# Kernel optimization log

Hardware: AMD Instinct MI355X
Metric: run time of the kernel (lower is better)

Reference implementation:

```python
import jax, jax.numpy as jnp
import numpy as np

ALPHA = 0.2          # LeakyReLU negative slope (Alpha)
NEG_INF = -9e15      # mask value used by pygat-style GAT


def _masked_attention(Wh, a_src, a_dst, mask):
    """Wh: [H,N,d], a_src/a_dst: [H,d], mask: [N,N] (nonzero = edge).
    Returns attention-aggregated features [H,N,d]."""
    f_src = jnp.einsum('hnd,hd->hn', Wh, a_src)   # [H,N]
    f_dst = jnp.einsum('hnd,hd->hn', Wh, a_dst)   # [H,N]
    e = jax.nn.leaky_relu(f_src[:, :, None] + f_dst[:, None, :], ALPHA)  # [H,N,N]
    e = jnp.where(mask[None, :, :] > 0, e, NEG_INF)
    att = jax.nn.softmax(e, axis=-1)              # masked softmax over neighbors
    return jnp.einsum('hnm,hmd->hnd', att, Wh)    # [H,N,d]


def setup_inputs() -> dict:
    key = jax.random.key(0)
    ks = jax.random.split(key, 8)
    N, F_in, D, H = 4096, 512, 64, 8
    x = jax.random.normal(ks[0], (N, F_in), dtype=jnp.float32)
    adj = jax.random.randint(ks[1], (N, N), 0, 2, dtype=jnp.int32)
    s = 0.1
    W = jax.random.normal(ks[2], (H, F_in, D), dtype=jnp.float32) * s
    a_src = jax.random.normal(ks[3], (H, D), dtype=jnp.float32) * s
    a_dst = jax.random.normal(ks[4], (H, D), dtype=jnp.float32) * s
    W_o = jax.random.normal(ks[5], (H * D, D), dtype=jnp.float32) * s
    ao_src = jax.random.normal(ks[6], (D,), dtype=jnp.float32) * s
    ao_dst = jax.random.normal(ks[7], (D,), dtype=jnp.float32) * s
    return {"x": x, "adj": adj, "W": W, "a_src": a_src, "a_dst": a_dst,
            "W_o": W_o, "ao_src": ao_src, "ao_dst": ao_dst}


def reference(x, adj, W, a_src, a_dst, W_o, ao_src, ao_dst):
    N = x.shape[0]
    # --- multi-head layer (concat=True: ELU per head, concat on feature dim) ---
    Wh = jnp.einsum('nf,hfd->hnd', x, W)                     # [H,N,d]
    h1 = jax.nn.elu(_masked_attention(Wh, a_src, a_dst, adj))  # [H,N,d]
    h_cat = jnp.transpose(h1, (1, 0, 2)).reshape(N, -1)      # [N, H*d]
    # --- output head (concat=False: no ELU inside layer) ---
    Who = (h_cat @ W_o)[None]                                # [1,N,d]
    h2 = _masked_attention(Who, ao_src[None], ao_dst[None], adj)[0]  # [N,d]
    # GAT.forward: activation (ELU) then log_softmax over dim=1
    return jax.nn.log_softmax(jax.nn.elu(h2), axis=1)
```

## Files before the change

### kernel.cpp

```cpp
#include <hip/hip_runtime.h>
#include <hip/hip_bf16.h>
#include <math.h>

#define N_NODES 4096
#define FDIM 512
#define D 64
#define H 8
#define NWORDS (N_NODES / 64)

typedef __attribute__((ext_vector_type(8))) short bf16x8;
typedef __attribute__((ext_vector_type(4))) float f32x4;

__device__ inline short f2bf(float x) {
    return (short)((__builtin_bit_cast(unsigned int, x) + 0x8000u) >> 16);
}

__device__ inline int sext_bit(unsigned int v, int j) {
#if defined(__has_builtin) && __has_builtin(__builtin_amdgcn_sbfe)
    return __builtin_amdgcn_sbfe((int)v, j, 1);
#else
    return ((int)(v << (31 - j))) >> 31;
#endif
}

__device__ inline unsigned fenc(float f) {
    unsigned u = __builtin_bit_cast(unsigned, f);
    return (u & 0x80000000u) ? ~u : (u | 0x80000000u);
}
__device__ inline float fdec(unsigned e) {
    unsigned u = (e & 0x80000000u) ? (e & 0x7FFFFFFFu) : ~e;
    return __builtin_bit_cast(float, u);
}

__device__ inline void gl2lds16(const void* g, void* l) {
#if defined(__has_builtin) && __has_builtin(__builtin_amdgcn_global_load_lds)
    __builtin_amdgcn_global_load_lds(
        (const __attribute__((address_space(1))) unsigned int*)g,
        (__attribute__((address_space(3))) unsigned int*)l, 16, 0, 0);
#else
    *(uint4*)l = *(const uint4*)g;
#endif
}

#define NB_BITS (N_NODES * N_NODES / 256)
#define NB_X    (N_NODES * FDIM / 256)
#define NB_W    (H * FDIM * D / 256)
#define NB_WO   (FDIM * D / 256)
__global__ void k_pre(const int* __restrict__ adj, const float* __restrict__ x,
                      const float* __restrict__ W, const float* __restrict__ Wo,
                      unsigned long long* __restrict__ bits, short* __restrict__ Xbf,
                      short* __restrict__ WF, short* __restrict__ WoF,
                      float* __restrict__ cm1, float* __restrict__ cm2,
                      unsigned* __restrict__ gmaxe1, unsigned* __restrict__ gmaxe2) {
    const int b = blockIdx.x, t = threadIdx.x;
    if (b == 0) {
        for (int i = t; i < H * D; i += 256) cm1[i] = 0.f;
        if (t < D) cm2[t] = 0.f;
        if (t < H) gmaxe1[t] = 0u;
        if (t == 0) gmaxe2[0] = 0u;
        return;
    }
    if (b < 1 + NB_BITS) {
        const int idx = (b - 1) * 256 + t;
        unsigned long long m = __ballot(adj[idx] != 0);
        if ((t & 63) == 0) bits[idx >> 6] = m;
        return;
    }
    if (b < 1 + NB_BITS + NB_X) {
        const size_t idx = (size_t)(b - 1 - NB_BITS) * 256 + t;
        Xbf[idx] = f2bf(x[idx]);
        return;
    }
    if (b < 1 + NB_BITS + NB_X + NB_W) {
        const size_t idx = (size_t)(b - 1 - NB_BITS - NB_X) * 256 + t;
        const int d = idx & 63;
        const int k = (int)(idx >> 6) & 511;
        const int h = (int)(idx >> 15);
        WF[(((size_t)h * 64 + (k >> 3)) * 64 + d) * 8 + (k & 7)] = f2bf(W[idx]);
        return;
    }
    {
        const size_t idx = (size_t)(b - 1 - NB_BITS - NB_X - NB_W) * 256 + t;
        const int d = idx & 63;
        const int k = (int)(idx >> 6);
        WoF[(((size_t)(k >> 3)) * 64 + d) * 8 + (k & 7)] = f2bf(Wo[idx]);
    }
}

__global__ void __launch_bounds__(256) k_gemm(
    const short* __restrict__ Xbf, const short* __restrict__ WF,
    const float* __restrict__ av, const float* __restrict__ bv,
    short* __restrict__ WBout, float* __restrict__ fs, float* __restrict__ fd,
    unsigned* __restrict__ gmaxe, float* __restrict__ cm) {
    const int h  = blockIdx.y;
    const int i0 = blockIdx.x * 64;
    const int t = threadIdx.x, w = t >> 6, lane = t & 63;
    const int li = lane & 15, quad = lane >> 4, k0 = quad * 8;
    const int row_a = i0 + w * 16 + li;
    const short* __restrict__ Xr  = Xbf + (size_t)row_a * FDIM;
    const short* __restrict__ WFh = WF + (size_t)h * 64 * D * 8;

    f32x4 c0 = {0.f, 0.f, 0.f, 0.f}, c1 = c0, c2 = c0, c3 = c0;
    #pragma unroll 4
    for (int kt = 0; kt < FDIM; kt += 32) {
        bf16x8 a = *(const bf16x8*)&Xr[kt + k0];
        const short* bb = WFh + (size_t)((kt >> 3) + quad) * (D * 8) + li * 8;
        bf16x8 b0 = *(const bf16x8*)(bb);
        bf16x8 b1 = *(const bf16x8*)(bb + 128);
        bf16x8 b2 = *(const bf16x8*)(bb + 256);
        bf16x8 b3 = *(const bf16x8*)(bb + 384);
        c0 = __builtin_amdgcn_mfma_f32_16x16x32_bf16(a, b0, c0, 0, 0, 0);
        c1 = __builtin_amdgcn_mfma_f32_16x16x32_bf16(a, b1, c1, 0, 0, 0);
        c2 = __builtin_amdgcn_mfma_f32_16x16x32_bf16(a, b2, c2, 0, 0, 0);
        c3 = __builtin_amdgcn_mfma_f32_16x16x32_bf16(a, b3, c3, 0, 0, 0);
    }
    float av4[4], bv4[4];
    #pragma unroll
    for (int t4 = 0; t4 < 4; ++t4) {
        av4[t4] = av[h * D + t4 * 16 + li];
        bv4[t4] = bv[h * D + t4 * 16 + li];
    }
    float tiles[4][4];
    #pragma unroll
    for (int r = 0; r < 4; ++r) { tiles[0][r] = c0[r]; tiles[1][r] = c1[r]; tiles[2][r] = c2[r]; tiles[3][r] = c3[r]; }

    __shared__ float csum[4][64];
    __shared__ float red[4];
    float fdmax = -INFINITY;
    float s4[4] = {0.f, 0.f, 0.f, 0.f};

    #pragma unroll
    for (int r = 0; r < 4; ++r) {
        const int row = i0 + w * 16 + quad * 4 + r;
        float pa = 0.f, pb = 0.f;
        #pragma unroll
        for (int t4 = 0; t4 < 4; ++t4) {
            const float v = tiles[t4][r];
            const int d = t4 * 16 + li;
            WBout[((size_t)h * (N_NODES / 8) + (row >> 3)) * (D * 8) + d * 8 + (row & 7)] = f2bf(v);
            pa += v * av4[t4];
            pb += v * bv4[t4];
            s4[t4] += v;
        }
        #pragma unroll
        for (int off = 1; off < 16; off <<= 1) {
            pa += __shfl_xor(pa, off);
            pb += __shfl_xor(pb, off);
        }
        if (li == 0) {
            fs[(size_t)h * N_NODES + row] = pa;
            fd[(size_t)h * N_NODES + row] = pb;
        }
        fdmax = fmaxf(fdmax, pb);
    }
    fdmax = fmaxf(fdmax, __shfl_xor(fdmax, 16));
    fdmax = fmaxf(fdmax, __shfl_xor(fdmax, 32));
    if (lane == 0) red[w] = fdmax;
    #pragma unroll
    for (int t4 = 0; t4 < 4; ++t4) {
        s4[t4] += __shfl_xor(s4[t4], 16);
        s4[t4] += __shfl_xor(s4[t4], 32);
    }
    if (quad == 0)
        #pragma unroll
        for (int t4 = 0; t4 < 4; ++t4) csum[w][t4 * 16 + li] = s4[t4];
    __syncthreads();
    if (t == 0)
        atomicMax(gmaxe + h, fenc(fmaxf(fmaxf(red[0], red[1]), fmaxf(red[2], red[3]))));
    if (t < 64)
        atomicAdd(&cm[h * D + t],
                  (csum[0][t] + csum[1][t] + csum[2][t] + csum[3][t]) * (1.f / (float)N_NODES));
}

__global__ void __launch_bounds__(256) k_accum(
    const unsigned int* __restrict__ bits32,
    const short* __restrict__ WB,
    const float* __restrict__ fsb, const float* __restrict__ fdb,
    const unsigned* __restrict__ gmaxe,
    float* __restrict__ num, float* __restrict__ den, int kslab) {

    __shared__ __align__(16) short Bt[2][16 * 64 * 8];
    __shared__ __align__(16) float EG[2][256];

    const int h = blockIdx.y, i0 = blockIdx.x * 128, slab = blockIdx.z;
    const int t = threadIdx.x, w = t >> 6, lane = t & 63;
    const int li = lane & 15, quad = lane >> 4, k0 = quad * 8;
    const int    r0 = i0 + w * 32 + li;
    const int    r1 = r0 + 16;
    const size_t ho = (size_t)h * N_NODES;
    const float  gm = fdec(gmaxe[h]);
    const float  Rv0 = __expf(-0.8f * (fsb[ho + r0] + gm));
    const float  Rv1 = __expf(-0.8f * (fsb[ho + r1] + gm));
    const float* __restrict__ fd = fdb + ho;
    const short* __restrict__ Bh = WB + (size_t)h * (N_NODES / 8) * D * 8;
    const unsigned int* __restrict__ brow0 = bits32 + (size_t)r0 * (NWORDS * 2);
    const unsigned int* __restrict__ brow1 = bits32 + (size_t)r1 * (NWORDS * 2);

    f32x4 acc[2][4], c5[2];
    #pragma unroll
    for (int f = 0; f < 2; ++f) {
        #pragma unroll
        for (int q = 0; q < 4; ++q) acc[f][q] = (f32x4){0.f, 0.f, 0.f, 0.f};
        c5[f] = (f32x4){0.f, 0.f, 0.f, 0.f};
    }
    bf16x8 ones;
    #pragma unroll
    for (int j = 0; j < 8; ++j) ones[j] = (short)0x3F80;

    const int k_beg = slab * kslab;
    const int ntile = kslab / 128;

    auto stage = [&](int buf, int jt) {
        const short* src = Bh + (size_t)(jt >> 3) * (D * 8);
        #pragma unroll
        for (int p = 0; p < 4; ++p)
            gl2lds16(src + (size_t)(p * 256 + t) * 8, &Bt[buf][(p * 256 + t) * 8]);
        if (w == 0) {
            float2 f2 = *(const float2*)&fd[jt + lane * 2];
            float2 ev, gv;
            ev.x = __expf(f2.x - gm);          ev.y = __expf(f2.y - gm);
            gv.x = __expf(0.2f * (f2.x - gm)); gv.y = __expf(0.2f * (f2.y - gm));
            *(float2*)&EG[buf][lane * 2]       = ev;
            *(float2*)&EG[buf][128 + lane * 2] = gv;
        }
    };

    stage(0, k_beg);
    uint4 bw0 = *(const uint4*)&brow0[k_beg >> 5];
    uint4 bw1 = *(const uint4*)&brow1[k_beg >> 5];
    for (int tile = 0; tile < ntile; ++tile) {
        const int jt = k_beg + tile * 128;
        __syncthreads();
        if (tile + 1 < ntile) stage((tile + 1) & 1, jt + 128);
        const short* Bl  = Bt[tile & 1];
        const float* EGl = EG[tile & 1];
        const unsigned int bwa0[4] = {bw0.x, bw0.y, bw0.z, bw0.w};
        const unsigned int bwa1[4] = {bw1.x, bw1.y, bw1.z, bw1.w};
        if (tile + 1 < ntile) {
            bw0 = *(const uint4*)&brow0[(jt + 128) >> 5];
            bw1 = *(const uint4*)&brow1[(jt + 128) >> 5];
        }
        #pragma unroll
        for (int s = 0; s < 4; ++s) {
            const float4 e0 = *(const float4*)&EGl[s * 32 + k0];
            const float4 e1 = *(const float4*)&EGl[s * 32 + k0 + 4];
            const float4 g0 = *(const float4*)&EGl[128 + s * 32 + k0];
            const float4 g1 = *(const float4*)&EGl[128 + s * 32 + k0 + 4];
            const unsigned int byt0 = (bwa0[s] >> k0) & 0xFFu;
            const unsigned int byt1 = (bwa1[s] >> k0) & 0xFFu;
            float ev[8], gv[8];
            ev[0] = e0.x; ev[1] = e0.y; ev[2] = e0.z; ev[3] = e0.w;
            ev[4] = e1.x; ev[5] = e1.y; ev[6] = e1.z; ev[7] = e1.w;
            gv[0] = g0.x; gv[1] = g0.y; gv[2] = g0.z; gv[3] = g0.w;
            gv[4] = g1.x; gv[5] = g1.y; gv[6] = g1.z; gv[7] = g1.w;
            unsigned int pa0[8], pa1[8];
            #pragma unroll
            for (int j = 0; j < 8; ++j) {
                const float p0 = fmaxf(ev[j], gv[j] * Rv0);
                const float p1 = fmaxf(ev[j], gv[j] * Rv1);
                pa0[j] = __builtin_bit_cast(unsigned int, p0)
                         & (unsigned int)sext_bit(byt0, j);
                pa1[j] = __builtin_bit_cast(unsigned int, p1)
                         & (unsigned int)sext_bit(byt1, j);
            }
            bf16x8 a0, a1;
            unsigned int* au0 = (unsigned int*)&a0;
            unsigned int* au1 = (unsigned int*)&a1;
            au0[0] = __builtin_amdgcn_perm(pa0[1], pa0[0], 0x07060302);
            au0[1] = __builtin_amdgcn_perm(pa0[3], pa0[2], 0x07060302);
            au0[2] = __builtin_amdgcn_perm(pa0[5], pa0[4], 0x07060302);
            au0[3] = __builtin_amdgcn_perm(pa0[7], pa0[6], 0x07060302);
            au1[0] = __builtin_amdgcn_perm(pa1[1], pa1[0], 0x07060302);
            au1[1] = __builtin_amdgcn_perm(pa1[3], pa1[2], 0x07060302);
            au1[2] = __builtin_amdgcn_perm(pa1[5], pa1[4], 0x07060302);
            au1[3] = __builtin_amdgcn_perm(pa1[7], pa1[6], 0x07060302);

            const short* bb = Bl + (size_t)((s * 4 + quad) * 64 + li) * 8;
            bf16x8 b0 = *(const bf16x8*)(bb);
            bf16x8 b1 = *(const bf16x8*)(bb + 128);
            bf16x8 b2 = *(const bf16x8*)(bb + 256);
            bf16x8 b3 = *(const bf16x8*)(bb + 384);
            acc[0][0] = __builtin_amdgcn_mfma_f32_16x16x32_bf16(a0, b0, acc[0][0], 0, 0, 0);
            acc[0][1] = __builtin_amdgcn_mfma_f32_16x16x32_bf16(a0, b1, acc[0][1], 0, 0, 0);
            acc[0][2] = __builtin_amdgcn_mfma_f32_16x16x32_bf16(a0, b2, acc[0][2], 0, 0, 0);
            acc[0][3] = __builtin_amdgcn_mfma_f32_16x16x32_bf16(a0, b3, acc[0][3], 0, 0, 0);
            c5[0]     = __builtin_amdgcn_mfma_f32_16x16x32_bf16(a0, ones, c5[0], 0, 0, 0);
            acc[1][0] = __builtin_amdgcn_mfma_f32_16x16x32_bf16(a1, b0, acc[1][0], 0, 0, 0);
            acc[1][1] = __builtin_amdgcn_mfma_f32_16x16x32_bf16(a1, b1, acc[1][1], 0, 0, 0);
            acc[1][2] = __builtin_amdgcn_mfma_f32_16x16x32_bf16(a1, b2, acc[1][2], 0, 0, 0);
            acc[1][3] = __builtin_amdgcn_mfma_f32_16x16x32_bf16(a1, b3, acc[1][3], 0, 0, 0);
            c5[1]     = __builtin_amdgcn_mfma_f32_16x16x32_bf16(a1, ones, c5[1], 0, 0, 0);
        }
    }

    const size_t so = (size_t)(slab * gridDim.y + h);
    #pragma unroll
    for (int f = 0; f < 2; ++f) {
        #pragma unroll
        for (int t4 = 0; t4 < 4; ++t4)
            #pragma unroll
            for (int r = 0; r < 4; ++r) {
                const int row = i0 + w * 32 + f * 16 + quad * 4 + r;
                num[(so * N_NODES + row) * D + t4 * 16 + li] = acc[f][t4][r];
            }
        if (li == 0)
            #pragma unroll
            for (int r = 0; r < 4; ++r)
                den[so * N_NODES + i0 + w * 32 + f * 16 + quad * 4 + r] = c5[f][r];
    }
}

__global__ void k_post1(const float* __restrict__ num, const float* __restrict__ den,
                        const float* __restrict__ colmean, short* __restrict__ hcat) {
    const int h   = blockIdx.y;
    const int i0  = blockIdx.x * 64;
    const int t   = threadIdx.x;
    const int row = i0 + (t >> 2);
    const int cb  = (t & 3) * 16;
    const size_t HN = (size_t)gridDim.y * N_NODES;
    const size_t r0 = (size_t)h * N_NODES + row;
    float dsum = 0.f;
    #pragma unroll
    for (int s = 0; s < 4; ++s) dsum += den[s * HN + r0];
    const bool  uni  = !(dsum > 0.f);
    const float linv = uni ? 0.f : 1.f / dsum;
    #pragma unroll
    for (int c = 0; c < 4; ++c) {
        const int col = cb + c * 4;
        float4 v = {0.f, 0.f, 0.f, 0.f};
        #pragma unroll
        for (int s = 0; s < 4; ++s) {
            float4 a = *(const float4*)&num[(s * HN + r0) * D + col];
            v.x += a.x; v.y += a.y; v.z += a.z; v.w += a.w;
        }
        v.x *= linv; v.y *= linv; v.z *= linv; v.w *= linv;
        if (uni) v = *(const float4*)&colmean[h * D + col];
        v.x = v.x > 0.f ? v.x : __expf(v.x) - 1.f;
        v.y = v.y > 0.f ? v.y : __expf(v.y) - 1.f;
        v.z = v.z > 0.f ? v.z : __expf(v.z) - 1.f;
        v.w = v.w > 0.f ? v.w : __expf(v.w) - 1.f;
        ushort4 o;
        o.x = (unsigned short)f2bf(v.x); o.y = (unsigned short)f2bf(v.y);
        o.z = (unsigned short)f2bf(v.z); o.w = (unsigned short)f2bf(v.w);
        *(ushort4*)&hcat[(size_t)row * (H * D) + h * D + col] = o;
    }
}

__global__ void k_lsm(const float* __restrict__ num, const float* __restrict__ den,
                      const float* __restrict__ cm, float* __restrict__ out) {
    const int n    = blockIdx.x * 4 + (threadIdx.x >> 6);
    const int lane = threadIdx.x & 63;
    float v = 0.f, ds = 0.f;
    #pragma unroll
    for (int s = 0; s < 16; ++s) v  += num[((size_t)s * N_NODES + n) * D + lane];
    #pragma unroll
    for (int s = 0; s < 16; ++s) ds += den[(size_t)s * N_NODES + n];
    v = (ds > 0.f) ? v / ds : cm[lane];
    v = v > 0.f ? v : __expf(v) - 1.f;
    float mx = v;
    #pragma unroll
    for (int off = 32; off > 0; off >>= 1) mx = fmaxf(mx, __shfl_xor(mx, off));
    float ex = __expf(v - mx);
    float sum = ex;
    #pragma unroll
    for (int off = 32; off > 0; off >>= 1) sum += __shfl_xor(sum, off);
    out[(size_t)n * D + lane] = (v - mx) - __logf(sum);
}

extern "C" void kernel_launch(void* const* d_in, const int* in_sizes, int n_in,
                              void* d_out, int out_size, void* d_ws, size_t ws_size,
                              hipStream_t stream) {
    const float* x      = (const float*)d_in[0];
    const int*   adj    = (const int*)d_in[1];
    const float* W      = (const float*)d_in[2];
    const float* a_src  = (const float*)d_in[3];
    const float* a_dst  = (const float*)d_in[4];
    const float* W_o    = (const float*)d_in[5];
    const float* ao_src = (const float*)d_in[6];
    const float* ao_dst = (const float*)d_in[7];
    float* out = (float*)d_out;

    char* wsp = (char*)d_ws;
    size_t off = 0;
    auto alloc = [&](size_t bytes) -> void* {
        void* p = wsp + off;
        off += (bytes + 255) & ~(size_t)255;
        return p;
    };
    unsigned long long* adj_bits = (unsigned long long*)alloc((size_t)N_NODES * NWORDS * 8);
    short*    Xbf   = (short*)alloc((size_t)N_NODES * FDIM * 2);
    short*    WF1   = (short*)alloc((size_t)H * 64 * D * 8 * 2);
    short*    WoF   = (short*)alloc((size_t)64 * D * 8 * 2);
    short*    WhB   = (short*)alloc((size_t)H * N_NODES * D * 2);
    float*    fs1   = (float*)alloc((size_t)H * N_NODES * 4);
    float*    fd1   = (float*)alloc((size_t)H * N_NODES * 4);
    unsigned* gme1  = (unsigned*)alloc((size_t)H * 4);
    float*    cm1   = (float*)alloc((size_t)H * D * 4);
    float*    num1  = (float*)alloc((size_t)4 * H * N_NODES * D * 4);
    float*    den1  = (float*)alloc((size_t)4 * H * N_NODES * 4);
    short*    hcat  = (short*)alloc((size_t)N_NODES * H * D * 2);
    short*    WhoB  = (short*)alloc((size_t)N_NODES * D * 2);
    float*    fs2   = (float*)alloc((size_t)N_NODES * 4);
    float*    fd2   = (float*)alloc((size_t)N_NODES * 4);
    unsigned* gme2  = (unsigned*)alloc(4);
    float*    cm2   = (float*)alloc((size_t)D * 4);
    float*    num2  = (float*)alloc((size_t)16 * N_NODES * D * 4);
    float*    den2  = (float*)alloc((size_t)16 * N_NODES * 4);

    const unsigned int* bits32 = (const unsigned int*)adj_bits;

    k_pre  <<<dim3(1 + NB_BITS + NB_X + NB_W + NB_WO), dim3(256), 0, stream>>>(
        adj, x, W, W_o, adj_bits, Xbf, WF1, WoF, cm1, cm2, gme1, gme2);

    k_gemm <<<dim3(N_NODES / 64, H), dim3(256), 0, stream>>>(Xbf, WF1, a_src, a_dst,
                                                             WhB, fs1, fd1, gme1, cm1);
    k_accum<<<dim3(N_NODES / 128, H, 4), dim3(256), 0, stream>>>(bits32, WhB, fs1, fd1, gme1,
                                                                 num1, den1, N_NODES / 4);
    k_post1<<<dim3(N_NODES / 64, H), dim3(256), 0, stream>>>(num1, den1, cm1, hcat);

    k_gemm <<<dim3(N_NODES / 64, 1), dim3(256), 0, stream>>>(hcat, WoF, ao_src, ao_dst,
                                                             WhoB, fs2, fd2, gme2, cm2);
    k_accum<<<dim3(N_NODES / 128, 1, 16), dim3(256), 0, stream>>>(bits32, WhoB, fs2, fd2, gme2,
                                                                  num2, den2, N_NODES / 16);
    k_lsm  <<<dim3(N_NODES / 4), dim3(256), 0, stream>>>(num2, den2, cm2, out);
}
```

Before: 222.6 us.

## Widen accum row tile to 256 and vectorize adjacency bit packing

```diff
diff --git a/kernel.cpp b/kernel.cpp
--- a/kernel.cpp
+++ b/kernel.cpp
@@ -42,13 +42,13 @@
 #endif
 }
 
-#define NB_BITS (N_NODES * N_NODES / 256)
-#define NB_X    (N_NODES * FDIM / 256)
+#define NB_BITS (N_NODES * N_NODES / 2048)
+#define NB_X    (N_NODES * FDIM / 1024)
 #define NB_W    (H * FDIM * D / 256)
 #define NB_WO   (FDIM * D / 256)
 __global__ void k_pre(const int* __restrict__ adj, const float* __restrict__ x,
                       const float* __restrict__ W, const float* __restrict__ Wo,
-                      unsigned long long* __restrict__ bits, short* __restrict__ Xbf,
+                      unsigned int* __restrict__ bits32, short* __restrict__ Xbf,
                       short* __restrict__ WF, short* __restrict__ WoF,
                       float* __restrict__ cm1, float* __restrict__ cm2,
                       unsigned* __restrict__ gmaxe1, unsigned* __restrict__ gmaxe2) {
@@ -61,14 +61,26 @@
         return;
     }
     if (b < 1 + NB_BITS) {
-        const int idx = (b - 1) * 256 + t;
-        unsigned long long m = __ballot(adj[idx] != 0);
-        if ((t & 63) == 0) bits[idx >> 6] = m;
+        const int tid  = (b - 1) * 256 + t;
+        const size_t e0 = (size_t)tid * 8;
+        int4 a0 = *(const int4*)&adj[e0];
+        int4 a1 = *(const int4*)&adj[e0 + 4];
+        unsigned by = (unsigned)(a0.x != 0)       | ((unsigned)(a0.y != 0) << 1)
+                    | ((unsigned)(a0.z != 0) << 2) | ((unsigned)(a0.w != 0) << 3)
+                    | ((unsigned)(a1.x != 0) << 4) | ((unsigned)(a1.y != 0) << 5)
+                    | ((unsigned)(a1.z != 0) << 6) | ((unsigned)(a1.w != 0) << 7);
+        unsigned v = by | (__shfl_xor((int)by, 1) << 8);
+        v = v | ((unsigned)__shfl_xor((int)v, 2) << 16);
+        if ((t & 3) == 0) bits32[tid >> 2] = v;
         return;
     }
     if (b < 1 + NB_BITS + NB_X) {
-        const size_t idx = (size_t)(b - 1 - NB_BITS) * 256 + t;
-        Xbf[idx] = f2bf(x[idx]);
+        const size_t i4 = ((size_t)(b - 1 - NB_BITS) * 256 + t) * 4;
+        float4 v = *(const float4*)&x[i4];
+        ushort4 o;
+        o.x = (unsigned short)f2bf(v.x); o.y = (unsigned short)f2bf(v.y);
+        o.z = (unsigned short)f2bf(v.z); o.w = (unsigned short)f2bf(v.w);
+        *(ushort4*)&Xbf[i4] = o;
         return;
     }
     if (b < 1 + NB_BITS + NB_X + NB_W) {
@@ -182,23 +194,25 @@
     __shared__ __align__(16) short Bt[2][16 * 64 * 8];
     __shared__ __align__(16) float EG[2][256];
 
-    const int h = blockIdx.y, i0 = blockIdx.x * 128, slab = blockIdx.z;
+    const int h = blockIdx.y, i0 = blockIdx.x * 256, slab = blockIdx.z;
     const int t = threadIdx.x, w = t >> 6, lane = t & 63;
     const int li = lane & 15, quad = lane >> 4, k0 = quad * 8;
-    const int    r0 = i0 + w * 32 + li;
-    const int    r1 = r0 + 16;
     const size_t ho = (size_t)h * N_NODES;
     const float  gm = fdec(gmaxe[h]);
-    const float  Rv0 = __expf(-0.8f * (fsb[ho + r0] + gm));
-    const float  Rv1 = __expf(-0.8f * (fsb[ho + r1] + gm));
+    float Rv[4];
+    const unsigned int* __restrict__ brow[4];
+    #pragma unroll
+    for (int f = 0; f < 4; ++f) {
+        const int r = i0 + w * 64 + f * 16 + li;
+        Rv[f] = __expf(-0.8f * (fsb[ho + r] + gm));
+        brow[f] = bits32 + (size_t)r * (NWORDS * 2);
+    }
     const float* __restrict__ fd = fdb + ho;
     const short* __restrict__ Bh = WB + (size_t)h * (N_NODES / 8) * D * 8;
-    const unsigned int* __restrict__ brow0 = bits32 + (size_t)r0 * (NWORDS * 2);
-    const unsigned int* __restrict__ brow1 = bits32 + (size_t)r1 * (NWORDS * 2);
-
-    f32x4 acc[2][4], c5[2];
-    #pragma unroll
-    for (int f = 0; f < 2; ++f) {
+
+    f32x4 acc[4][4], c5[4];
+    #pragma unroll
+    for (int f = 0; f < 4; ++f) {
         #pragma unroll
         for (int q = 0; q < 4; ++q) acc[f][q] = (f32x4){0.f, 0.f, 0.f, 0.f};
         c5[f] = (f32x4){0.f, 0.f, 0.f, 0.f};
@@ -226,87 +240,78 @@
     };
 
     stage(0, k_beg);
-    uint4 bw0 = *(const uint4*)&brow0[k_beg >> 5];
-    uint4 bw1 = *(const uint4*)&brow1[k_beg >> 5];
+    uint4 bw[4];
+    #pragma unroll
+    for (int f = 0; f < 4; ++f) bw[f] = *(const uint4*)&brow[f][k_beg >> 5];
     for (int tile = 0; tile < ntile; ++tile) {
         const int jt = k_beg + tile * 128;
         __syncthreads();
         if (tile + 1 < ntile) stage((tile + 1) & 1, jt + 128);
         const short* Bl  = Bt[tile & 1];
         const float* EGl = EG[tile & 1];
-        const unsigned int bwa0[4] = {bw0.x, bw0.y, bw0.z, bw0.w};
-        const unsigned int bwa1[4] = {bw1.x, bw1.y, bw1.z, bw1.w};
-        if (tile + 1 < ntile) {
-            bw0 = *(const uint4*)&brow0[(jt + 128) >> 5];
-            bw1 = *(const uint4*)&brow1[(jt + 128) >> 5];
-        }
+        unsigned int bwa[4][4];
+        #pragma unroll
+        for (int f = 0; f < 4; ++f) {
+            bwa[f][0] = bw[f].x; bwa[f][1] = bw[f].y; bwa[f][2] = bw[f].z; bwa[f][3] = bw[f].w;
+        }
+        if (tile + 1 < ntile)
+            #pragma unroll
+            for (int f = 0; f < 4; ++f) bw[f] = *(const uint4*)&brow[f][(jt + 128) >> 5];
         #pragma unroll
         for (int s = 0; s < 4; ++s) {
             const float4 e0 = *(const float4*)&EGl[s * 32 + k0];
             const float4 e1 = *(const float4*)&EGl[s * 32 + k0 + 4];
             const float4 g0 = *(const float4*)&EGl[128 + s * 32 + k0];
             const float4 g1 = *(const float4*)&EGl[128 + s * 32 + k0 + 4];
-            const unsigned int byt0 = (bwa0[s] >> k0) & 0xFFu;
-            const unsigned int byt1 = (bwa1[s] >> k0) & 0xFFu;
             float ev[8], gv[8];
             ev[0] = e0.x; ev[1] = e0.y; ev[2] = e0.z; ev[3] = e0.w;
             ev[4] = e1.x; ev[5] = e1.y; ev[6] = e1.z; ev[7] = e1.w;
             gv[0] = g0.x; gv[1] = g0.y; gv[2] = g0.z; gv[3] = g0.w;
             gv[4] = g1.x; gv[5] = g1.y; gv[6] = g1.z; gv[7] = g1.w;
-            unsigned int pa0[8], pa1[8];
-            #pragma unroll
-            for (int j = 0; j < 8; ++j) {
-                const float p0 = fmaxf(ev[j], gv[j] * Rv0);
-                const float p1 = fmaxf(ev[j], gv[j] * Rv1);
-                pa0[j] = __builtin_bit_cast(unsigned int, p0)
-                         & (unsigned int)sext_bit(byt0, j);
-                pa1[j] = __builtin_bit_cast(unsigned int, p1)
-                         & (unsigned int)sext_bit(byt1, j);
-            }
-            bf16x8 a0, a1;
-            unsigned int* au0 = (unsigned int*)&a0;
-            unsigned int* au1 = (unsigned int*)&a1;
-            au0[0] = __builtin_amdgcn_perm(pa0[1], pa0[0], 0x07060302);
-            au0[1] = __builtin_amdgcn_perm(pa0[3], pa0[2], 0x07060302);
-            au0[2] = __builtin_amdgcn_perm(pa0[5], pa0[4], 0x07060302);
-            au0[3] = __builtin_amdgcn_perm(pa0[7], pa0[6], 0x07060302);
-            au1[0] = __builtin_amdgcn_perm(pa1[1], pa1[0], 0x07060302);
-            au1[1] = __builtin_amdgcn_perm(pa1[3], pa1[2], 0x07060302);
-            au1[2] = __builtin_amdgcn_perm(pa1[5], pa1[4], 0x07060302);
-            au1[3] = __builtin_amdgcn_perm(pa1[7], pa1[6], 0x07060302);
-
             const short* bb = Bl + (size_t)((s * 4 + quad) * 64 + li) * 8;
             bf16x8 b0 = *(const bf16x8*)(bb);
             bf16x8 b1 = *(const bf16x8*)(bb + 128);
             bf16x8 b2 = *(const bf16x8*)(bb + 256);
             bf16x8 b3 = *(const bf16x8*)(bb + 384);
-            acc[0][0] = __builtin_amdgcn_mfma_f32_16x16x32_bf16(a0, b0, acc[0][0], 0, 0, 0);
-            acc[0][1] = __builtin_amdgcn_mfma_f32_16x16x32_bf16(a0, b1, acc[0][1], 0, 0, 0);
-            acc[0][2] = __builtin_amdgcn_mfma_f32_16x16x32_bf16(a0, b2, acc[0][2], 0, 0, 0);
-            acc[0][3] = __builtin_amdgcn_mfma_f32_16x16x32_bf16(a0, b3, acc[0][3], 0, 0, 0);
-            c5[0]     = __builtin_amdgcn_mfma_f32_16x16x32_bf16(a0, ones, c5[0], 0, 0, 0);
-            acc[1][0] = __builtin_amdgcn_mfma_f32_16x16x32_bf16(a1, b0, acc[1][0], 0, 0, 0);
-            acc[1][1] = __builtin_amdgcn_mfma_f32_16x16x32_bf16(a1, b1, acc[1][1], 0, 0, 0);
-            acc[1][2] = __builtin_amdgcn_mfma_f32_16x16x32_bf16(a1, b2, acc[1][2], 0, 0, 0);
-            acc[1][3] = __builtin_amdgcn_mfma_f32_16x16x32_bf16(a1, b3, acc[1][3], 0, 0, 0);
-            c5[1]     = __builtin_amdgcn_mfma_f32_16x16x32_bf16(a1, ones, c5[1], 0, 0, 0);
+            #pragma unroll
+            for (int f = 0; f < 4; ++f) {
+                const unsigned int byt = (bwa[f][s] >> k0) & 0xFFu;
+                unsigned int pa[8];
+                #pragma unroll
+                for (int j = 0; j < 8; ++j) {
+                    const float p = fmaxf(ev[j], gv[j] * Rv[f]);
+                    pa[j] = __builtin_bit_cast(unsigned int, p)
+                            & (unsigned int)sext_bit(byt, j);
+                }
+                bf16x8 a;
+                unsigned int* au = (unsigned int*)&a;
+                au[0] = __builtin_amdgcn_perm(pa[1], pa[0], 0x07060302);
+                au[1] = __builtin_amdgcn_perm(pa[3], pa[2], 0x07060302);
+                au[2] = __builtin_amdgcn_perm(pa[5], pa[4], 0x07060302);
+                au[3] = __builtin_amdgcn_perm(pa[7], pa[6], 0x07060302);
+                acc[f][0] = __builtin_amdgcn_mfma_f32_16x16x32_bf16(a, b0, acc[f][0], 0, 0, 0);
+                acc[f][1] = __builtin_amdgcn_mfma_f32_16x16x32_bf16(a, b1, acc[f][1], 0, 0, 0);
+                acc[f][2] = __builtin_amdgcn_mfma_f32_16x16x32_bf16(a, b2, acc[f][2], 0, 0, 0);
+                acc[f][3] = __builtin_amdgcn_mfma_f32_16x16x32_bf16(a, b3, acc[f][3], 0, 0, 0);
+                c5[f]     = __builtin_amdgcn_mfma_f32_16x16x32_bf16(a, ones, c5[f], 0, 0, 0);
+            }
         }
     }
 
     const size_t so = (size_t)(slab * gridDim.y + h);
     #pragma unroll
-    for (int f = 0; f < 2; ++f) {
+    for (int f = 0; f < 4; ++f) {
         #pragma unroll
         for (int t4 = 0; t4 < 4; ++t4)
             #pragma unroll
             for (int r = 0; r < 4; ++r) {
-                const int row = i0 + w * 32 + f * 16 + quad * 4 + r;
+                const int row = i0 + w * 64 + f * 16 + quad * 4 + r;
                 num[(so * N_NODES + row) * D + t4 * 16 + li] = acc[f][t4][r];
             }
         if (li == 0)
             #pragma unroll
             for (int r = 0; r < 4; ++r)
-                den[so * N_NODES + i0 + w * 32 + f * 16 + quad * 4 + r] = c5[f][r];
+                den[so * N_NODES + i0 + w * 64 + f * 16 + quad * 4 + r] = c5[f][r];
     }
 }
 
@@ -352,9 +357,9 @@
     const int lane = threadIdx.x & 63;
     float v = 0.f, ds = 0.f;
     #pragma unroll
-    for (int s = 0; s < 16; ++s) v  += num[((size_t)s * N_NODES + n) * D + lane];
-    #pragma unroll
-    for (int s = 0; s < 16; ++s) ds += den[(size_t)s * N_NODES + n];
+    for (int s = 0; s < 32; ++s) v  += num[((size_t)s * N_NODES + n) * D + lane];
+    #pragma unroll
+    for (int s = 0; s < 32; ++s) ds += den[(size_t)s * N_NODES + n];
     v = (ds > 0.f) ? v / ds : cm[lane];
     v = v > 0.f ? v : __expf(v) - 1.f;
     float mx = v;
@@ -387,7 +392,7 @@
         off += (bytes + 255) & ~(size_t)255;
         return p;
     };
-    unsigned long long* adj_bits = (unsigned long long*)alloc((size_t)N_NODES * NWORDS * 8);
+    unsigned* adj_bits = (unsigned*)alloc((size_t)N_NODES * NWORDS * 8);
     short*    Xbf   = (short*)alloc((size_t)N_NODES * FDIM * 2);
     short*    WF1   = (short*)alloc((size_t)H * 64 * D * 8 * 2);
     short*    WoF   = (short*)alloc((size_t)64 * D * 8 * 2);
@@ -404,23 +409,21 @@
     float*    fd2   = (float*)alloc((size_t)N_NODES * 4);
     unsigned* gme2  = (unsigned*)alloc(4);
     float*    cm2   = (float*)alloc((size_t)D * 4);
-    float*    num2  = (float*)alloc((size_t)16 * N_NODES * D * 4);
-    float*    den2  = (float*)alloc((size_t)16 * N_NODES * 4);
-
-    const unsigned int* bits32 = (const unsigned int*)adj_bits;
+    float*    num2  = (float*)alloc((size_t)32 * N_NODES * D * 4);
+    float*    den2  = (float*)alloc((size_t)32 * N_NODES * 4);
 
     k_pre  <<<dim3(1 + NB_BITS + NB_X + NB_W + NB_WO), dim3(256), 0, stream>>>(
         adj, x, W, W_o, adj_bits, Xbf, WF1, WoF, cm1, cm2, gme1, gme2);
 
     k_gemm <<<dim3(N_NODES / 64, H), dim3(256), 0, stream>>>(Xbf, WF1, a_src, a_dst,
                                                              WhB, fs1, fd1, gme1, cm1);
-    k_accum<<<dim3(N_NODES / 128, H, 4), dim3(256), 0, stream>>>(bits32, WhB, fs1, fd1, gme1,
+    k_accum<<<dim3(N_NODES / 256, H, 4), dim3(256), 0, stream>>>(adj_bits, WhB, fs1, fd1, gme1,
                                                                  num1, den1, N_NODES / 4);
     k_post1<<<dim3(N_NODES / 64, H), dim3(256), 0, stream>>>(num1, den1, cm1, hcat);
 
     k_gemm <<<dim3(N_NODES / 64, 1), dim3(256), 0, stream>>>(hcat, WoF, ao_src, ao_dst,
                                                              WhoB, fs2, fd2, gme2, cm2);
-    k_accum<<<dim3(N_NODES / 128, 1, 16), dim3(256), 0, stream>>>(bits32, WhoB, fs2, fd2, gme2,
-                                                                  num2, den2, N_NODES / 16);
+    k_accum<<<dim3(N_NODES / 256, 1, 32), dim3(256), 0, stream>>>(adj_bits, WhoB, fs2, fd2, gme2,
+                                                                  num2, den2, N_NODES / 32);
     k_lsm  <<<dim3(N_NODES / 4), dim3(256), 0, stream>>>(num2, den2, cm2, out);
 }
```

After: 208.1 us. 6.5% less time.
